# Optimization experiments

Measured on AMD Instinct MI355X. Metric: run time of the kernel, lower is better.

The kernel has to match this reference:

```python
import jax, jax.numpy as jnp
import numpy as np
import math

B, S, D, H = 4, 2048, 512, 8
HD = D // H

def setup_inputs() -> dict:
    key = jax.random.key(0)
    ks = jax.random.split(key, 12)
    s_hd = 1.0 / math.sqrt(HD)
    s_d = 1.0 / math.sqrt(D)
    return {
        "q": jax.random.normal(ks[0], (B, S, D), jnp.float32),
        "k": jax.random.normal(ks[1], (B, S, D), jnp.float32),
        "v": jax.random.normal(ks[2], (B, S, D), jnp.float32),
        # torch nn.Linear(head_dim, head_dim): weight [HD, HD], bias [HD]
        "Wq": jax.random.uniform(ks[3], (HD, HD), jnp.float32, -s_hd, s_hd),
        "bq": jax.random.uniform(ks[4], (HD,), jnp.float32, -s_hd, s_hd),
        "Wk": jax.random.uniform(ks[5], (HD, HD), jnp.float32, -s_hd, s_hd),
        "bk": jax.random.uniform(ks[6], (HD,), jnp.float32, -s_hd, s_hd),
        "Wv": jax.random.uniform(ks[7], (HD, HD), jnp.float32, -s_hd, s_hd),
        "bv": jax.random.uniform(ks[8], (HD,), jnp.float32, -s_hd, s_hd),
        # output projection nn.Linear(d, d)
        "Wo": jax.random.uniform(ks[9], (D, D), jnp.float32, -s_d, s_d),
        "bo": jax.random.uniform(ks[10], (D,), jnp.float32, -s_d, s_d),
        # LayerNorm(d) affine params
        "gamma": jnp.ones((D,), jnp.float32),
        "beta": jnp.zeros((D,), jnp.float32),
    }

def _layernorm(x, gamma, beta, eps=1e-5):
    mu = jnp.mean(x, axis=-1, keepdims=True)
    var = jnp.var(x, axis=-1, keepdims=True)
    return (x - mu) * jax.lax.rsqrt(var + eps) * gamma + beta

def reference(q, k, v, Wq, bq, Wk, bk, Wv, bv, Wo, bo, gamma, beta):
    batch, q_len = q.shape[0], q.shape[1]
    # split heads: [B, L, H, HD]; per-head Linear shares one weight across heads
    Qh = q.reshape(batch, q_len, H, HD) @ Wq.T + bq
    Kh = k.reshape(batch, k.shape[1], H, HD) @ Wk.T + bk
    Vh = v.reshape(batch, v.shape[1], H, HD) @ Wv.T + bv
    # scores scaled by sqrt(d) (faithful to source, NOT sqrt(head_dim))
    scores = jnp.einsum('bqhd,bkhd->bhqk', Qh, Kh) / math.sqrt(D)
    attn = jax.nn.softmax(scores, axis=-1)
    out = jnp.einsum('bhqk,bkhd->bqhd', attn, Vh)
    concat = out.reshape(batch, q_len, D)
    lin = concat @ Wo.T + bo
    # AddNorm quirk: residual added AFTER LayerNorm (dropout = identity in eval)
    return q + _layernorm(lin, gamma, beta)
```

## Files before the change

### kernel.cpp

```cpp
#include <hip/hip_runtime.h>
#include <hip/hip_bf16.h>
#include <math.h>
#include <stdint.h>

#define B 4
#define S 2048
#define D 512
#define H 8
#define HD 64

typedef __attribute__((ext_vector_type(4))) int   int4v;
typedef __attribute__((ext_vector_type(8))) short short8;
typedef __attribute__((ext_vector_type(4))) short short4v;
typedef __attribute__((ext_vector_type(4))) float f32x4;

__device__ __forceinline__ unsigned short bfr(float x) {
    __bf16 h = (__bf16)x;
    union { __bf16 b; unsigned short s; } u; u.b = h; return u.s;
}
__device__ __forceinline__ float b2f(unsigned short s) {
    union { unsigned u; float f; } v; v.u = (unsigned)s << 16; return v.f;
}
__device__ __forceinline__ float ex2(float x) {
#if __has_builtin(__builtin_amdgcn_exp2f)
    return __builtin_amdgcn_exp2f(x);
#else
    return exp2f(x);
#endif
}
__device__ __forceinline__ short8 cvt8(const float* p) {
    float4 f0 = *(const float4*)p;
    float4 f1 = *(const float4*)(p + 4);
    short8 s8;
    s8[0] = (short)bfr(f0.x); s8[1] = (short)bfr(f0.y);
    s8[2] = (short)bfr(f0.z); s8[3] = (short)bfr(f0.w);
    s8[4] = (short)bfr(f1.x); s8[5] = (short)bfr(f1.y);
    s8[6] = (short)bfr(f1.z); s8[7] = (short)bfr(f1.w);
    return s8;
}

#define QSCALE 0.06377229601488305f
#define MFIX 4.0f

typedef const __attribute__((address_space(1))) unsigned char g8_t;
typedef __attribute__((address_space(3))) unsigned char l8_t;
__device__ __forceinline__ void gl_lds16(const unsigned short* g, unsigned short* l) {
#if __has_builtin(__builtin_amdgcn_global_load_lds)
    __builtin_amdgcn_global_load_lds((g8_t*)g, (l8_t*)l, 16, 0, 0);
#else
    int lane = threadIdx.x & 63;
    ((int4v*)l)[lane] = *(const int4v*)g;
#endif
}

__global__ __launch_bounds__(256) void qkv_mfma_kernel(
    const float* __restrict__ q, const float* __restrict__ k,
    const float* __restrict__ v,
    const float* __restrict__ Wq, const float* __restrict__ bq,
    const float* __restrict__ Wk, const float* __restrict__ bk,
    const float* __restrict__ Wv, const float* __restrict__ bv,
    const float* __restrict__ Wo, unsigned short* __restrict__ WoB,
    unsigned short* __restrict__ Qh, unsigned short* __restrict__ Kh,
    unsigned short* __restrict__ VtG)
{
    const int t = threadIdx.x;
    const int bid = blockIdx.x;
    if (bid >= 1536) {
        int i = (bid - 1536) * 1024 + t * 4;
        float4 f = *(const float4*)(Wo + i);
        short4v s;
        s[0] = (short)bfr(f.x); s[1] = (short)bfr(f.y);
        s[2] = (short)bfr(f.z); s[3] = (short)bfr(f.w);
        *(short4v*)(WoB + i) = s;
        return;
    }

    __shared__ __align__(16) unsigned short Wl[64 * 72];

    const int x   = bid / 512;
    const int r_  = bid - x * 512;
    const int bh  = r_ >> 4;
    const int stg = r_ & 15;
    const int b = bh >> 3, h = bh & 7;
    const int L = t & 63, w = t >> 6;
    const int c = L & 15, qd = L >> 4;

    const float* Wf     = (x == 0) ? Wq : (x == 1) ? Wk : Wv;
    const float* bias_p = (x == 0) ? bq : (x == 1) ? bk : bv;
    const float* X      = (x == 0) ? q  : (x == 1) ? k  : v;

    {
        int base = t * 16;
        int row = t >> 2, col = (t & 3) * 16;
        short8 s0 = cvt8(Wf + base);
        short8 s1 = cvt8(Wf + base + 8);
        *(short8*)&Wl[row * 72 + col]     = s0;
        *(short8*)&Wl[row * 72 + col + 8] = s1;
    }
    __syncthreads();

    short8 wf[4][2];
    #pragma unroll
    for (int nt = 0; nt < 4; ++nt)
        #pragma unroll
        for (int kc = 0; kc < 2; ++kc)
            wf[nt][kc] = *(const short8*)&Wl[(16 * nt + c) * 72 + kc * 32 + 8 * qd];

    if (x < 2) {
        float bias[4];
        #pragma unroll
        for (int nt = 0; nt < 4; ++nt) bias[nt] = bias_p[16 * nt + c];
        const float sc = (x == 0) ? QSCALE : 1.0f;
        #pragma unroll
        for (int ti = 0; ti < 2; ++ti) {
            const int st = stg * 8 + w * 2 + ti;
            const float* xrow = X + ((size_t)(b * S + st * 16 + c)) * D + h * HD;
            short8 af0 = cvt8(xrow + 8 * qd);
            short8 af1 = cvt8(xrow + 32 + 8 * qd);
            f32x4 acc[4];
            #pragma unroll
            for (int nt = 0; nt < 4; ++nt) {
                acc[nt] = (f32x4){bias[nt], bias[nt], bias[nt], bias[nt]};
                acc[nt] = __builtin_amdgcn_mfma_f32_16x16x32_bf16(af0, wf[nt][0], acc[nt], 0, 0, 0);
                acc[nt] = __builtin_amdgcn_mfma_f32_16x16x32_bf16(af1, wf[nt][1], acc[nt], 0, 0, 0);
            }
            unsigned short* O = ((x == 0) ? Qh : Kh)
                              + ((size_t)(b * H + h) * S + st * 16) * HD;
            #pragma unroll
            for (int nt = 0; nt < 4; ++nt)
                #pragma unroll
                for (int r = 0; r < 4; ++r)
                    O[(4 * qd + r) * HD + 16 * nt + c] = bfr(acc[nt][r] * sc);
        }
    } else {
        f32x4 bias4[4];
        #pragma unroll
        for (int nt = 0; nt < 4; ++nt) {
            float4 bb4 = *(const float4*)(bias_p + 16 * nt + 4 * qd);
            bias4[nt] = (f32x4){bb4.x, bb4.y, bb4.z, bb4.w};
        }
        #pragma unroll
        for (int ti = 0; ti < 2; ++ti) {
            const int st = stg * 8 + w * 2 + ti;
            const float* xrow = X + ((size_t)(b * S + st * 16 + c)) * D + h * HD;
            short8 af0 = cvt8(xrow + 8 * qd);
            short8 af1 = cvt8(xrow + 32 + 8 * qd);
            f32x4 acc[4];
            #pragma unroll
            for (int nt = 0; nt < 4; ++nt) {
                acc[nt] = bias4[nt];
                acc[nt] = __builtin_amdgcn_mfma_f32_16x16x32_bf16(wf[nt][0], af0, acc[nt], 0, 0, 0);
                acc[nt] = __builtin_amdgcn_mfma_f32_16x16x32_bf16(wf[nt][1], af1, acc[nt], 0, 0, 0);
            }
            unsigned short* O = VtG + (size_t)(b * H + h) * HD * S;
            #pragma unroll
            for (int nt = 0; nt < 4; ++nt)
                #pragma unroll
                for (int r = 0; r < 4; ++r)
                    O[(size_t)(16 * nt + 4 * qd + r) * S + st * 16 + c] = bfr(acc[nt][r]);
        }
    }
}

__global__ __launch_bounds__(256, 4) void attn_kernel(
    const unsigned short* __restrict__ Qh, const unsigned short* __restrict__ Kh,
    const unsigned short* __restrict__ VtG, unsigned short* __restrict__ accPb,
    float* __restrict__ lP)
{
    __shared__ __align__(16) unsigned short Ks[2][4096];
    __shared__ __align__(16) unsigned short Vs[2][4096];

    const int idx = blockIdx.x;
    const int bh = idx & 31;
    const int rem = idx >> 5;
    const int qt = rem >> 1;
    const int ks = rem & 1;
    const int b = bh >> 3, h = bh & 7;
    const int t = threadIdx.x;
    const int w = t >> 6, L = t & 63;
    const int c = L & 15, qd = L >> 4;

    const unsigned short* Kb = Kh + ((size_t)bh * S + ks * 1024) * HD;
    const unsigned short* Vb = VtG + (size_t)bh * HD * S + ks * 1024;

    short8 qf[2][2];
    #pragma unroll
    for (int qg = 0; qg < 2; ++qg)
        #pragma unroll
        for (int kc = 0; kc < 2; ++kc)
            qf[qg][kc] = *(const short8*)(Qh
                + ((size_t)bh * S + qt * 128 + w * 32 + qg * 16 + c) * HD
                + kc * 32 + 8 * qd);

    f32x4 acc[2][4];
    float lrun[2] = {0.f, 0.f};
    #pragma unroll
    for (int qg = 0; qg < 2; ++qg)
        #pragma unroll
        for (int dt = 0; dt < 4; ++dt) acc[qg][dt] = (f32x4){0.f, 0.f, 0.f, 0.f};

    const int sd = t >> 3, sj = t & 7;
    const int sp = sj >> 2, smt = (sj >> 1) & 1;
    const int sqa = (2 * sj) & 3, sqb = (2 * sj + 1) & 3;

    int4v vpre[2];
    #pragma unroll
    for (int i = 0; i < 2; ++i) {
        int bi = w + 4 * i;
        gl_lds16(Kb + (size_t)(16 * (bi >> 1) + c) * HD + (bi & 1) * 32 + qd * 8,
                 &Ks[0][bi * 512]);
        vpre[i] = *(const int4v*)(Vb + (size_t)(sd + 32 * i) * S + 8 * sj);
    }

    for (int it = 0; it < 16; ++it) {
        const int cur = it & 1, nxt = cur ^ 1;
        #pragma unroll
        for (int i = 0; i < 2; ++i) {
            int d = sd + 32 * i;
            int dt = d >> 4, cc = d & 15;
            union { int4v v; short4v h[2]; } u; u.v = vpre[i];
            *(short4v*)&Vs[cur][((dt * 2 + sp) * 64 + sqa * 16 + cc) * 8 + smt * 4] = u.h[0];
            *(short4v*)&Vs[cur][((dt * 2 + sp) * 64 + sqb * 16 + cc) * 8 + smt * 4] = u.h[1];
        }
        __syncthreads();
        if (it + 1 < 16) {
            int n1 = (it + 1) * 64;
            #pragma unroll
            for (int i = 0; i < 2; ++i) {
                int bi = w + 4 * i;
                gl_lds16(Kb + (size_t)(n1 + 16 * (bi >> 1) + c) * HD + (bi & 1) * 32 + qd * 8,
                         &Ks[nxt][bi * 512]);
                vpre[i] = *(const int4v*)(Vb + (size_t)(sd + 32 * i) * S + n1 + 8 * sj);
            }
        }

        const unsigned short* KsC = Ks[cur];
        const unsigned short* VsC = Vs[cur];

        short4v pa[2][4];
        #pragma unroll
        for (int mt = 0; mt < 4; ++mt) {
            short8 a0 = *(const short8*)(KsC + (mt * 2 + 0) * 512 + L * 8);
            short8 a1 = *(const short8*)(KsC + (mt * 2 + 1) * 512 + L * 8);
            #pragma unroll
            for (int qg = 0; qg < 2; ++qg) {
                f32x4 stv = (f32x4){-MFIX, -MFIX, -MFIX, -MFIX};
                stv = __builtin_amdgcn_mfma_f32_16x16x32_bf16(a0, qf[qg][0], stv, 0, 0, 0);
                stv = __builtin_amdgcn_mfma_f32_16x16x32_bf16(a1, qf[qg][1], stv, 0, 0, 0);
                float p0 = ex2(stv[0]), p1 = ex2(stv[1]);
                float p2 = ex2(stv[2]), p3 = ex2(stv[3]);
                lrun[qg] += (p0 + p1) + (p2 + p3);
                short4v p_;
                p_[0] = (short)bfr(p0); p_[1] = (short)bfr(p1);
                p_[2] = (short)bfr(p2); p_[3] = (short)bfr(p3);
                pa[qg][mt] = p_;
            }
        }

        #pragma unroll
        for (int dt = 0; dt < 4; ++dt)
            #pragma unroll
            for (int p = 0; p < 2; ++p) {
                union { short8 v8; short4v h[2]; } u;
                u.v8 = *(const short8*)(VsC + (dt * 2 + p) * 512 + L * 8);
#if __has_builtin(__builtin_amdgcn_mfma_f32_16x16x16bf16_1k)
                #pragma unroll
                for (int qg = 0; qg < 2; ++qg) {
                    acc[qg][dt] = __builtin_amdgcn_mfma_f32_16x16x16bf16_1k(
                        pa[qg][2 * p + 0], u.h[0], acc[qg][dt], 0, 0, 0);
                    acc[qg][dt] = __builtin_amdgcn_mfma_f32_16x16x16bf16_1k(
                        pa[qg][2 * p + 1], u.h[1], acc[qg][dt], 0, 0, 0);
                }
#else
                #pragma unroll
                for (int qg = 0; qg < 2; ++qg) {
                    short8 pz0 = {pa[qg][2 * p + 0][0], pa[qg][2 * p + 0][1],
                                  pa[qg][2 * p + 0][2], pa[qg][2 * p + 0][3], 0, 0, 0, 0};
                    short8 pz1 = {pa[qg][2 * p + 1][0], pa[qg][2 * p + 1][1],
                                  pa[qg][2 * p + 1][2], pa[qg][2 * p + 1][3], 0, 0, 0, 0};
                    short8 v0 = {u.h[0][0], u.h[0][1], u.h[0][2], u.h[0][3], 0, 0, 0, 0};
                    short8 v1 = {u.h[1][0], u.h[1][1], u.h[1][2], u.h[1][3], 0, 0, 0, 0};
                    acc[qg][dt] = __builtin_amdgcn_mfma_f32_16x16x32_bf16(pz0, v0, acc[qg][dt], 0, 0, 0);
                    acc[qg][dt] = __builtin_amdgcn_mfma_f32_16x16x32_bf16(pz1, v1, acc[qg][dt], 0, 0, 0);
                }
#endif
            }
    }

    const int q0 = qt * 128 + w * 32;
    unsigned short* accPp = accPb + (size_t)ks * ((size_t)B * S * D)
                          + ((size_t)b * S + q0) * D + h * HD;
    #pragma unroll
    for (int qg = 0; qg < 2; ++qg) {
        float lr = lrun[qg];
        lr += __shfl_xor(lr, 16);
        lr += __shfl_xor(lr, 32);
        if (qd == 0)
            lP[(size_t)ks * ((size_t)B * H * S) + (size_t)bh * S + q0 + qg * 16 + c] = lr;
        #pragma unroll
        for (int dt = 0; dt < 4; ++dt)
            #pragma unroll
            for (int r = 0; r < 4; ++r)
                accPp[(size_t)(qg * 16 + 4 * qd + r) * D + 16 * dt + c]
                    = bfr(acc[qg][dt][r]);
    }
}

__global__ __launch_bounds__(1024) void oproj_ln_kernel(
    const unsigned short* __restrict__ accPb, const float* __restrict__ lP,
    const unsigned short* __restrict__ WoB,
    const float* __restrict__ bo, const float* __restrict__ gamma,
    const float* __restrict__ beta, const float* __restrict__ qin,
    float* __restrict__ out)
{
    __shared__ __align__(16) unsigned short As[32 * 520];
    __shared__ float red[2][32][17];
    __shared__ float linv_s[32][8];
    __shared__ float mu_s2[32], rs_s2[32];

    const int t = threadIdx.x;
    const int r0 = blockIdx.x * 32;
    const int w = t >> 6, L = t & 63;
    const int c = L & 15, qd = L >> 4;
    const int n0 = w * 32;
    const size_t NEh = (size_t)B * S * D;
    const size_t BHS = (size_t)B * H * S;

    if (t < 256) {
        int row = t >> 3, hh = t & 7;
        int bb = r0 >> 11;
        int ss = (r0 & (S - 1)) + row;
        float l0 = lP[(size_t)(bb * H + hh) * S + ss];
        float l1 = lP[BHS + (size_t)(bb * H + hh) * S + ss];
        linv_s[row][hh] = 1.f / (l0 + l1);
    }
    __syncthreads();

    #pragma unroll
    for (int i = 0; i < 4; ++i) {
        int flat = t + 1024 * i;
        int row = flat >> 7, cg = flat & 127;
        int col = cg * 4;
        size_t gi = (size_t)(r0 + row) * D + col;
        short4v a0 = *(const short4v*)(accPb + gi);
        short4v a1 = *(const short4v*)(accPb + NEh + gi);
        float li = linv_s[row][col >> 6];
        short4v s;
        #pragma unroll
        for (int j = 0; j < 4; ++j)
            s[j] = (short)bfr((b2f((unsigned short)a0[j])
                             + b2f((unsigned short)a1[j])) * li);
        *(short4v*)&As[row * 520 + col] = s;
    }
    __syncthreads();

    f32x4 acc[2][2];
    #pragma unroll
    for (int nt = 0; nt < 2; ++nt) {
        float bv_ = bo[n0 + 16 * nt + c];
        acc[0][nt] = (f32x4){bv_, bv_, bv_, bv_};
        acc[1][nt] = (f32x4){bv_, bv_, bv_, bv_};
    }

    for (int kc = 0; kc < 16; ++kc) {
        short8 a0 = *(const short8*)&As[c * 520 + kc * 32 + 8 * qd];
        short8 a1 = *(const short8*)&As[(16 + c) * 520 + kc * 32 + 8 * qd];
        #pragma unroll
        for (int nt = 0; nt < 2; ++nt) {
            short8 bf = *(const short8*)(WoB + (size_t)(n0 + 16 * nt + c) * D
                                         + kc * 32 + 8 * qd);
            acc[0][nt] = __builtin_amdgcn_mfma_f32_16x16x32_bf16(a0, bf, acc[0][nt], 0, 0, 0);
            acc[1][nt] = __builtin_amdgcn_mfma_f32_16x16x32_bf16(a1, bf, acc[1][nt], 0, 0, 0);
        }
    }

    float sm[2][4], sq[2][4];
    #pragma unroll
    for (int mt = 0; mt < 2; ++mt)
        #pragma unroll
        for (int r = 0; r < 4; ++r) { sm[mt][r] = 0.f; sq[mt][r] = 0.f; }
    #pragma unroll
    for (int mt = 0; mt < 2; ++mt)
        #pragma unroll
        for (int nt = 0; nt < 2; ++nt)
            #pragma unroll
            for (int r = 0; r < 4; ++r) {
                float x_ = acc[mt][nt][r];
                sm[mt][r] += x_; sq[mt][r] += x_ * x_;
            }
    #pragma unroll
    for (int mask = 1; mask <= 8; mask <<= 1)
        #pragma unroll
        for (int mt = 0; mt < 2; ++mt)
            #pragma unroll
            for (int r = 0; r < 4; ++r) {
                sm[mt][r] += __shfl_xor(sm[mt][r], mask);
                sq[mt][r] += __shfl_xor(sq[mt][r], mask);
            }
    if (c == 0) {
        #pragma unroll
        for (int mt = 0; mt < 2; ++mt)
            #pragma unroll
            for (int r = 0; r < 4; ++r) {
                red[0][mt * 16 + 4 * qd + r][w] = sm[mt][r];
                red[1][mt * 16 + 4 * qd + r][w] = sq[mt][r];
            }
    }
    __syncthreads();

    if (t < 32) {
        float s_ = 0.f, q_ = 0.f;
        #pragma unroll
        for (int w_ = 0; w_ < 16; ++w_) { s_ += red[0][t][w_]; q_ += red[1][t][w_]; }
        float mu_ = s_ * (1.f / D);
        float var = q_ * (1.f / D) - mu_ * mu_;
        mu_s2[t] = mu_;
        rs_s2[t] = rsqrtf(var + 1e-5f);
    }
    __syncthreads();

    #pragma unroll
    for (int nt = 0; nt < 2; ++nt) {
        int n = n0 + 16 * nt + c;
        float g = gamma[n], be = beta[n];
        #pragma unroll
        for (int mt = 0; mt < 2; ++mt)
            #pragma unroll
            for (int r = 0; r < 4; ++r) {
                int m = mt * 16 + 4 * qd + r;
                size_t gi = (size_t)(r0 + m) * D + n;
                out[gi] = qin[gi] + (acc[mt][nt][r] - mu_s2[m]) * rs_s2[m] * g + be;
            }
    }
}

extern "C" void kernel_launch(void* const* d_in, const int* in_sizes, int n_in,
                              void* d_out, int out_size, void* d_ws, size_t ws_size,
                              hipStream_t stream) {
    const float* q     = (const float*)d_in[0];
    const float* k     = (const float*)d_in[1];
    const float* v     = (const float*)d_in[2];
    const float* Wq    = (const float*)d_in[3];
    const float* bq    = (const float*)d_in[4];
    const float* Wk    = (const float*)d_in[5];
    const float* bk    = (const float*)d_in[6];
    const float* Wv    = (const float*)d_in[7];
    const float* bv    = (const float*)d_in[8];
    const float* Wo    = (const float*)d_in[9];
    const float* bo    = (const float*)d_in[10];
    const float* gamma = (const float*)d_in[11];
    const float* beta  = (const float*)d_in[12];
    float* out = (float*)d_out;

    const size_t NE = (size_t)B * S * D;
    unsigned short* wsu = (unsigned short*)d_ws;
    unsigned short* Qh    = wsu;
    unsigned short* Kh    = wsu + NE;
    unsigned short* VtG   = wsu + 2 * NE;
    unsigned short* WoB   = wsu + 3 * NE;
    unsigned short* accPb = WoB + (size_t)D * D;
    float* lP = (float*)(accPb + 2 * NE);

    hipLaunchKernelGGL(qkv_mfma_kernel, dim3(1536 + 256), dim3(256), 0, stream,
                       q, k, v, Wq, bq, Wk, bk, Wv, bv, Wo, WoB, Qh, Kh, VtG);
    hipLaunchKernelGGL(attn_kernel, dim3(1024), dim3(256), 0, stream,
                       Qh, Kh, VtG, accPb, lP);
    hipLaunchKernelGGL(oproj_ln_kernel, dim3(B * S / 32), dim3(1024), 0, stream,
                       accPb, lP, WoB, bo, gamma, beta, q, out);
}
```

Measured before the change: 192.5 us.

## Fuse QKV, attention and output projection into one cooperative persistent kernel

Replaces the three separate launches (QKV projection, split-K attention, out-projection plus LayerNorm) with a single cooperative kernel of 1024 blocks that uses grid-wide syncs between phases. The O-projection phase is restructured to 16-row tiles over 512 blocks with an XOR-swizzled LDS layout. The aim is to remove launch gaps and per-kernel tail effects. In exchange it introduces grid-sync cost, a fixed 16KB shared buffer, and occupancy constraints (launch_bounds 256,4), and it falls back to the old path if the cooperative launch is not possible.

```diff
diff --git a/kernel.cpp b/kernel.cpp
--- a/kernel.cpp
+++ b/kernel.cpp
@@ -1,7 +1,10 @@
 #include <hip/hip_runtime.h>
+#include <hip/hip_cooperative_groups.h>
 #include <hip/hip_bf16.h>
 #include <math.h>
 #include <stdint.h>
+
+namespace cg = cooperative_groups;
 
 #define B 4
 #define S 2048
@@ -51,6 +54,326 @@
     int lane = threadIdx.x & 63;
     ((int4v*)l)[lane] = *(const int4v*)g;
 #endif
+}
+
+__global__ __launch_bounds__(256, 4) void fused_kernel(
+    const float* __restrict__ q, const float* __restrict__ k,
+    const float* __restrict__ v,
+    const float* __restrict__ Wq, const float* __restrict__ bq,
+    const float* __restrict__ Wk, const float* __restrict__ bk,
+    const float* __restrict__ Wv, const float* __restrict__ bv,
+    const float* __restrict__ Wo, const float* __restrict__ bo,
+    const float* __restrict__ gamma, const float* __restrict__ beta,
+    unsigned short* __restrict__ Qh, unsigned short* __restrict__ Kh,
+    unsigned short* __restrict__ VtG, unsigned short* __restrict__ WoB,
+    unsigned short* __restrict__ accPb, float* __restrict__ lP,
+    float* __restrict__ out)
+{
+    __shared__ __align__(16) unsigned char smem[16384];
+
+    const int bid = blockIdx.x;
+    const int t = threadIdx.x;
+    const int w = t >> 6, L = t & 63;
+    const int c = L & 15, qd = L >> 4;
+    const size_t NEh = (size_t)B * S * D;
+    const size_t BHS = (size_t)B * H * S;
+
+    {
+        int wi = bid * 256 + t;
+        WoB[wi] = bfr(Wo[wi]);
+
+        const int bh = bid & 31;
+        const int sg = bid >> 5;
+        const int b = bh >> 3, h = bh & 7;
+        const int st = sg * 4 + w;
+        unsigned short* Wl = (unsigned short*)smem;
+
+        const float* Wsrc[3]  = {Wq, Wk, Wv};
+        const float* biasP[3] = {bq, bk, bv};
+        const float* Xs[3]    = {q, k, v};
+
+        for (int x = 0; x < 3; ++x) {
+            __syncthreads();
+            {
+                int row = t >> 2, col = (t & 3) * 16;
+                *(short8*)&Wl[row * 72 + col]     = cvt8(Wsrc[x] + t * 16);
+                *(short8*)&Wl[row * 72 + col + 8] = cvt8(Wsrc[x] + t * 16 + 8);
+            }
+            __syncthreads();
+
+            short8 wf[4][2];
+            #pragma unroll
+            for (int nt = 0; nt < 4; ++nt)
+                #pragma unroll
+                for (int kc = 0; kc < 2; ++kc)
+                    wf[nt][kc] = *(const short8*)&Wl[(16 * nt + c) * 72 + kc * 32 + 8 * qd];
+
+            const float* xrow = Xs[x] + ((size_t)(b * S + st * 16 + c)) * D + h * HD;
+            short8 af0 = cvt8(xrow + 8 * qd);
+            short8 af1 = cvt8(xrow + 32 + 8 * qd);
+
+            if (x < 2) {
+                f32x4 acc[4];
+                #pragma unroll
+                for (int nt = 0; nt < 4; ++nt) {
+                    float bv_ = biasP[x][16 * nt + c];
+                    acc[nt] = (f32x4){bv_, bv_, bv_, bv_};
+                    acc[nt] = __builtin_amdgcn_mfma_f32_16x16x32_bf16(af0, wf[nt][0], acc[nt], 0, 0, 0);
+                    acc[nt] = __builtin_amdgcn_mfma_f32_16x16x32_bf16(af1, wf[nt][1], acc[nt], 0, 0, 0);
+                }
+                unsigned short* O = ((x == 0) ? Qh : Kh)
+                                  + ((size_t)(b * H + h) * S + st * 16) * HD;
+                const float sc = (x == 0) ? QSCALE : 1.0f;
+                #pragma unroll
+                for (int nt = 0; nt < 4; ++nt)
+                    #pragma unroll
+                    for (int r = 0; r < 4; ++r)
+                        O[(4 * qd + r) * HD + 16 * nt + c] = bfr(acc[nt][r] * sc);
+            } else {
+                f32x4 acc[4];
+                #pragma unroll
+                for (int nt = 0; nt < 4; ++nt) {
+                    float4 bb4 = *(const float4*)(biasP[x] + 16 * nt + 4 * qd);
+                    acc[nt] = (f32x4){bb4.x, bb4.y, bb4.z, bb4.w};
+                    acc[nt] = __builtin_amdgcn_mfma_f32_16x16x32_bf16(wf[nt][0], af0, acc[nt], 0, 0, 0);
+                    acc[nt] = __builtin_amdgcn_mfma_f32_16x16x32_bf16(wf[nt][1], af1, acc[nt], 0, 0, 0);
+                }
+                unsigned short* O = VtG + (size_t)(b * H + h) * HD * S;
+                #pragma unroll
+                for (int nt = 0; nt < 4; ++nt)
+                    #pragma unroll
+                    for (int r = 0; r < 4; ++r)
+                        O[(size_t)(16 * nt + 4 * qd + r) * S + st * 16 + c] = bfr(acc[nt][r]);
+            }
+        }
+    }
+
+    cg::this_grid().sync();
+
+    {
+        unsigned short (*Ks)[4096] = (unsigned short (*)[4096])smem;
+
+        const int bh = bid & 31;
+        const int rem = bid >> 5;
+        const int qt = rem >> 1;
+        const int ks = rem & 1;
+        const int b = bh >> 3, h = bh & 7;
+
+        const unsigned short* Kb = Kh + ((size_t)bh * S + ks * 1024) * HD;
+        const unsigned short* Vb = VtG + (size_t)bh * HD * S + ks * 1024;
+
+        short8 qf[2][2];
+        #pragma unroll
+        for (int qg = 0; qg < 2; ++qg)
+            #pragma unroll
+            for (int kc = 0; kc < 2; ++kc)
+                qf[qg][kc] = *(const short8*)(Qh
+                    + ((size_t)bh * S + qt * 128 + w * 32 + qg * 16 + c) * HD
+                    + kc * 32 + 8 * qd);
+
+        f32x4 acc[2][4];
+        float lrun[2] = {0.f, 0.f};
+        #pragma unroll
+        for (int qg = 0; qg < 2; ++qg)
+            #pragma unroll
+            for (int dt = 0; dt < 4; ++dt) acc[qg][dt] = (f32x4){0.f, 0.f, 0.f, 0.f};
+
+        #pragma unroll
+        for (int i = 0; i < 2; ++i) {
+            int bi = w + 4 * i;
+            gl_lds16(Kb + (size_t)(16 * (bi >> 1) + c) * HD + (bi & 1) * 32 + qd * 8,
+                     &Ks[0][bi * 512]);
+        }
+
+        for (int it = 0; it < 16; ++it) {
+            const int cur = it & 1;
+            __syncthreads();
+            if (it + 1 < 16) {
+                int n1 = (it + 1) * 64;
+                #pragma unroll
+                for (int i = 0; i < 2; ++i) {
+                    int bi = w + 4 * i;
+                    gl_lds16(Kb + (size_t)(n1 + 16 * (bi >> 1) + c) * HD + (bi & 1) * 32 + qd * 8,
+                             &Ks[cur ^ 1][bi * 512]);
+                }
+            }
+            const int n0 = it * 64;
+
+            short4v vf[4][4];
+            #pragma unroll
+            for (int dt = 0; dt < 4; ++dt)
+                #pragma unroll
+                for (int mt = 0; mt < 4; ++mt)
+                    vf[dt][mt] = *(const short4v*)(Vb + (size_t)(16 * dt + c) * S
+                                                   + n0 + 16 * mt + 4 * qd);
+
+            const unsigned short* KsC = Ks[cur];
+            short4v pa[2][4];
+            #pragma unroll
+            for (int mt = 0; mt < 4; ++mt) {
+                short8 a0 = *(const short8*)(KsC + (mt * 2 + 0) * 512 + L * 8);
+                short8 a1 = *(const short8*)(KsC + (mt * 2 + 1) * 512 + L * 8);
+                #pragma unroll
+                for (int qg = 0; qg < 2; ++qg) {
+                    f32x4 stv = (f32x4){-MFIX, -MFIX, -MFIX, -MFIX};
+                    stv = __builtin_amdgcn_mfma_f32_16x16x32_bf16(a0, qf[qg][0], stv, 0, 0, 0);
+                    stv = __builtin_amdgcn_mfma_f32_16x16x32_bf16(a1, qf[qg][1], stv, 0, 0, 0);
+                    float p0 = ex2(stv[0]), p1 = ex2(stv[1]);
+                    float p2 = ex2(stv[2]), p3 = ex2(stv[3]);
+                    lrun[qg] += (p0 + p1) + (p2 + p3);
+                    short4v p_;
+                    p_[0] = (short)bfr(p0); p_[1] = (short)bfr(p1);
+                    p_[2] = (short)bfr(p2); p_[3] = (short)bfr(p3);
+                    pa[qg][mt] = p_;
+                }
+            }
+
+            #pragma unroll
+            for (int dt = 0; dt < 4; ++dt)
+                #pragma unroll
+                for (int mt = 0; mt < 4; ++mt) {
+#if __has_builtin(__builtin_amdgcn_mfma_f32_16x16x16bf16_1k)
+                    #pragma unroll
+                    for (int qg = 0; qg < 2; ++qg)
+                        acc[qg][dt] = __builtin_amdgcn_mfma_f32_16x16x16bf16_1k(
+                            pa[qg][mt], vf[dt][mt], acc[qg][dt], 0, 0, 0);
+#else
+                    #pragma unroll
+                    for (int qg = 0; qg < 2; ++qg) {
+                        short8 pz = {pa[qg][mt][0], pa[qg][mt][1],
+                                     pa[qg][mt][2], pa[qg][mt][3], 0, 0, 0, 0};
+                        short8 vz = {vf[dt][mt][0], vf[dt][mt][1],
+                                     vf[dt][mt][2], vf[dt][mt][3], 0, 0, 0, 0};
+                        acc[qg][dt] = __builtin_amdgcn_mfma_f32_16x16x32_bf16(pz, vz, acc[qg][dt], 0, 0, 0);
+                    }
+#endif
+                }
+        }
+
+        const int q0 = qt * 128 + w * 32;
+        unsigned short* accPp = accPb + (size_t)ks * NEh
+                              + ((size_t)b * S + q0) * D + h * HD;
+        #pragma unroll
+        for (int qg = 0; qg < 2; ++qg) {
+            float lr = lrun[qg];
+            lr += __shfl_xor(lr, 16);
+            lr += __shfl_xor(lr, 32);
+            if (qd == 0)
+                lP[(size_t)ks * BHS + (size_t)bh * S + q0 + qg * 16 + c] = lr;
+            #pragma unroll
+            for (int dt = 0; dt < 4; ++dt)
+                #pragma unroll
+                for (int r = 0; r < 4; ++r)
+                    accPp[(size_t)(qg * 16 + 4 * qd + r) * D + 16 * dt + c]
+                        = bfr(acc[qg][dt][r]);
+        }
+    }
+
+    cg::this_grid().sync();
+
+    if (bid < 512) {
+        unsigned short* As = (unsigned short*)smem;
+
+        const int r0 = bid * 16;
+        const int n0 = w * 128;
+        const int bb = r0 >> 11;
+
+        #pragma unroll
+        for (int i = 0; i < 8; ++i) {
+            int flat = t + 256 * i;
+            int row = flat >> 7, cg4 = flat & 127;
+            int col = cg4 * 4;
+            size_t gi = (size_t)(r0 + row) * D + col;
+            short4v a0 = *(const short4v*)(accPb + gi);
+            short4v a1 = *(const short4v*)(accPb + NEh + gi);
+            int hh = col >> 6, ss = (r0 & (S - 1)) + row;
+            float l0 = lP[(size_t)(bb * H + hh) * S + ss];
+            float l1 = lP[BHS + (size_t)(bb * H + hh) * S + ss];
+            float li = 1.f / (l0 + l1);
+            short4v s;
+            #pragma unroll
+            for (int j = 0; j < 4; ++j)
+                s[j] = (short)bfr((b2f((unsigned short)a0[j])
+                                 + b2f((unsigned short)a1[j])) * li);
+            int chunk8 = cg4 >> 1;
+            *(short4v*)&As[row * 512 + ((chunk8 ^ (row & 7)) << 3) + (cg4 & 1) * 4] = s;
+        }
+        __syncthreads();
+
+        f32x4 acc[8];
+        #pragma unroll
+        for (int nt = 0; nt < 8; ++nt) {
+            float bv_ = bo[n0 + 16 * nt + c];
+            acc[nt] = (f32x4){bv_, bv_, bv_, bv_};
+        }
+
+        for (int kc = 0; kc < 16; ++kc) {
+            short8 a0 = *(const short8*)&As[c * 512 + (((kc * 4 + qd) ^ (c & 7)) << 3)];
+            #pragma unroll
+            for (int nt = 0; nt < 8; ++nt) {
+                short8 bf = *(const short8*)(WoB + (size_t)(n0 + 16 * nt + c) * D
+                                             + kc * 32 + 8 * qd);
+                acc[nt] = __builtin_amdgcn_mfma_f32_16x16x32_bf16(a0, bf, acc[nt], 0, 0, 0);
+            }
+        }
+        __syncthreads();
+
+        float* red   = (float*)smem;
+        float* mu_s2 = (float*)(smem + 2048);
+        float* rs_s2 = (float*)(smem + 2048 + 64);
+
+        float sm[4], sq[4];
+        #pragma unroll
+        for (int r = 0; r < 4; ++r) { sm[r] = 0.f; sq[r] = 0.f; }
+        #pragma unroll
+        for (int nt = 0; nt < 8; ++nt)
+            #pragma unroll
+            for (int r = 0; r < 4; ++r) {
+                float x_ = acc[nt][r];
+                sm[r] += x_; sq[r] += x_ * x_;
+            }
+        #pragma unroll
+        for (int mask = 1; mask <= 8; mask <<= 1)
+            #pragma unroll
+            for (int r = 0; r < 4; ++r) {
+                sm[r] += __shfl_xor(sm[r], mask);
+                sq[r] += __shfl_xor(sq[r], mask);
+            }
+        if (c == 0) {
+            #pragma unroll
+            for (int r = 0; r < 4; ++r) {
+                red[w * 16 + 4 * qd + r]       = sm[r];
+                red[(4 + w) * 16 + 4 * qd + r] = sq[r];
+            }
+        }
+        __syncthreads();
+
+        if (t < 16) {
+            float s_ = 0.f, q_ = 0.f;
+            #pragma unroll
+            for (int w_ = 0; w_ < 4; ++w_) {
+                s_ += red[w_ * 16 + t];
+                q_ += red[(4 + w_) * 16 + t];
+            }
+            float mu_ = s_ * (1.f / D);
+            float var = q_ * (1.f / D) - mu_ * mu_;
+            mu_s2[t] = mu_;
+            rs_s2[t] = rsqrtf(var + 1e-5f);
+        }
+        __syncthreads();
+
+        #pragma unroll
+        for (int nt = 0; nt < 8; ++nt) {
+            int n = n0 + 16 * nt + c;
+            float g = gamma[n], be = beta[n];
+            #pragma unroll
+            for (int r = 0; r < 4; ++r) {
+                int m = 4 * qd + r;
+                size_t gi = (size_t)(r0 + m) * D + n;
+                out[gi] = q[gi] + (acc[nt][r] - mu_s2[m]) * rs_s2[m] * g + be;
+            }
+        }
+    }
 }
 
 __global__ __launch_bounds__(256) void qkv_mfma_kernel(
@@ -90,12 +413,9 @@
     const float* X      = (x == 0) ? q  : (x == 1) ? k  : v;
 
     {
-        int base = t * 16;
         int row = t >> 2, col = (t & 3) * 16;
-        short8 s0 = cvt8(Wf + base);
-        short8 s1 = cvt8(Wf + base + 8);
-        *(short8*)&Wl[row * 72 + col]     = s0;
-        *(short8*)&Wl[row * 72 + col + 8] = s1;
+        *(short8*)&Wl[row * 72 + col]     = cvt8(Wf + t * 16);
+        *(short8*)&Wl[row * 72 + col + 8] = cvt8(Wf + t * 16 + 8);
     }
     __syncthreads();
 
@@ -339,8 +659,8 @@
     #pragma unroll
     for (int i = 0; i < 4; ++i) {
         int flat = t + 1024 * i;
-        int row = flat >> 7, cg = flat & 127;
-        int col = cg * 4;
+        int row = flat >> 7, cg4 = flat & 127;
+        int col = cg4 * 4;
         size_t gi = (size_t)(r0 + row) * D + col;
         short4v a0 = *(const short4v*)(accPb + gi);
         short4v a1 = *(const short4v*)(accPb + NEh + gi);
@@ -461,10 +781,31 @@
     unsigned short* accPb = WoB + (size_t)D * D;
     float* lP = (float*)(accPb + 2 * NE);
 
-    hipLaunchKernelGGL(qkv_mfma_kernel, dim3(1536 + 256), dim3(256), 0, stream,
-                       q, k, v, Wq, bq, Wk, bk, Wv, bv, Wo, WoB, Qh, Kh, VtG);
-    hipLaunchKernelGGL(attn_kernel, dim3(1024), dim3(256), 0, stream,
-                       Qh, Kh, VtG, accPb, lP);
-    hipLaunchKernelGGL(oproj_ln_kernel, dim3(B * S / 32), dim3(1024), 0, stream,
-                       accPb, lP, WoB, bo, gamma, beta, q, out);
-}
+    int maxB = 0;
+    hipError_t qe = hipOccupancyMaxActiveBlocksPerMultiprocessor(
+        &maxB, (const void*)fused_kernel, 256, 0);
+    bool coop = (qe == hipSuccess && maxB >= 4);
+
+    if (coop) {
+        void* args[] = {
+            (void*)&q, (void*)&k, (void*)&v,
+            (void*)&Wq, (void*)&bq, (void*)&Wk, (void*)&bk, (void*)&Wv, (void*)&bv,
+            (void*)&Wo, (void*)&bo, (void*)&gamma, (void*)&beta,
+            (void*)&Qh, (void*)&Kh, (void*)&VtG, (void*)&WoB,
+            (void*)&accPb, (void*)&lP, (void*)&out
+        };
+        hipError_t rc = hipLaunchCooperativeKernel((const void*)fused_kernel,
+                                                   dim3(1024), dim3(256),
+                                                   args, 0, stream);
+        if (rc != hipSuccess) coop = false;
+    }
+
+    if (!coop) {
+        hipLaunchKernelGGL(qkv_mfma_kernel, dim3(1536 + 256), dim3(256), 0, stream,
+                           q, k, v, Wq, bq, Wk, bk, Wv, bv, Wo, WoB, Qh, Kh, VtG);
+        hipLaunchKernelGGL(attn_kernel, dim3(1024), dim3(256), 0, stream,
+                           Qh, Kh, VtG, accPb, lP);
+        hipLaunchKernelGGL(oproj_ln_kernel, dim3(B * S / 32), dim3(1024), 0, stream,
+                           accPb, lP, WoB, bo, gamma, beta, q, out);
+    }
+}
```

Result: no change. 190.7 us (-0.9%).
